# Kernel tuning notes

Measured on AMD Instinct MI355X. Metric: run time of the kernel, lower is better.

The kernel has to match this reference:

```python
import jax, jax.numpy as jnp
import numpy as np

QMAX = 127.0          # int8 symmetric range
MMA_ALPHA = 1024.0    # leap mmaAlpha; applied to one scale and removed from the other (net no-op)
EPS = 1e-12


def _dynamic_quantize(t):
    """Per-tensor (blockSize=-1) symmetric int8 dynamic quantization."""
    s = jnp.maximum(jnp.max(jnp.abs(t)) / QMAX, EPS)
    q = jnp.clip(jnp.round(t / s), -QMAX, QMAX).astype(jnp.int8)
    return q, s


def setup_inputs() -> dict:
    key = jax.random.key(0)
    k1, k2 = jax.random.split(key)
    x = jax.random.normal(k1, (8192, 256), dtype=jnp.float32)   # [M, K]
    y = jax.random.normal(k2, (256, 8192), dtype=jnp.float32)   # [K, N]
    return {"x": x, "y": y}


def reference(x, y):
    x_q, x_s = _dynamic_quantize(x)
    y_q, y_s = _dynamic_quantize(y)
    # Integer accumulation (K=256 * 127^2 fits easily in int32), then dequantize.
    acc = jnp.matmul(x_q.astype(jnp.int32), y_q.astype(jnp.int32))  # [M, N] int32
    # mmaAlpha rescaling: scale one operand's scale up by alpha, the other down; cancels exactly.
    out = acc.astype(jnp.float32) * ((x_s * MMA_ALPHA) * (y_s / MMA_ALPHA))
    return out
```

## Files before the change

### kernel.cpp

```cpp
#include <hip/hip_runtime.h>

#define M_DIM 8192
#define N_DIM 8192
#define K_DIM 256

typedef __attribute__((ext_vector_type(4))) int i32x4;
typedef __attribute__((ext_vector_type(4))) float f32x4;

__device__ __forceinline__ void bar_lds() {
    asm volatile("s_waitcnt lgkmcnt(0)" ::: "memory");
    __builtin_amdgcn_sched_barrier(0);
    __builtin_amdgcn_s_barrier();
}

__device__ __forceinline__ void bar_stage() {
    asm volatile("s_waitcnt vmcnt(0) lgkmcnt(0)" ::: "memory");
    __builtin_amdgcn_sched_barrier(0);
    __builtin_amdgcn_s_barrier();
}

__device__ __forceinline__ void async_lds16(const signed char* g, signed char* l) {
    __builtin_amdgcn_global_load_lds(
        (const __attribute__((address_space(1))) void*)g,
        (__attribute__((address_space(3))) void*)l, 16, 0, 0);
}

__global__ __launch_bounds__(256) void absmax_kernel(const float* __restrict__ x,
                                                     const float* __restrict__ y,
                                                     float* __restrict__ partial) {
    const float* p = (blockIdx.y == 0) ? x : y;
    const int n4 = (M_DIM * K_DIM) / 4;
    const float4* p4 = (const float4*)p;
    float m = 0.0f;
    for (int i = blockIdx.x * 256 + threadIdx.x; i < n4; i += 256 * 256) {
        float4 v = p4[i];
        m = fmaxf(m, fmaxf(fmaxf(fabsf(v.x), fabsf(v.y)), fmaxf(fabsf(v.z), fabsf(v.w))));
    }
    for (int off = 32; off > 0; off >>= 1)
        m = fmaxf(m, __shfl_down(m, off));
    __shared__ float sm[4];
    int wid = threadIdx.x >> 6;
    if ((threadIdx.x & 63) == 0) sm[wid] = m;
    __syncthreads();
    if (threadIdx.x == 0)
        partial[blockIdx.y * 256 + blockIdx.x] = fmaxf(fmaxf(sm[0], sm[1]), fmaxf(sm[2], sm[3]));
}

__device__ __forceinline__ void load_scales(const float* __restrict__ partial,
                                            float& sx, float& sy, float* ssc) {
    const int tid = threadIdx.x;
    float mx = partial[tid];
    float my = partial[256 + tid];
    for (int off = 32; off > 0; off >>= 1) {
        mx = fmaxf(mx, __shfl_down(mx, off));
        my = fmaxf(my, __shfl_down(my, off));
    }
    if ((tid & 63) == 0) { ssc[tid >> 6] = mx; ssc[4 + (tid >> 6)] = my; }
    __syncthreads();
    mx = fmaxf(fmaxf(ssc[0], ssc[1]), fmaxf(ssc[2], ssc[3]));
    my = fmaxf(fmaxf(ssc[4], ssc[5]), fmaxf(ssc[6], ssc[7]));
    sx = fmaxf(mx / 127.0f, 1e-12f);
    sy = fmaxf(my / 127.0f, 1e-12f);
}

__device__ __forceinline__ int quant1(float v, float s) {
    float q = rintf(v / s);
    q = fmaxf(-127.0f, fminf(127.0f, q));
    return (int)q;
}

__global__ __launch_bounds__(256) void quant_kernel(const float* __restrict__ x,
                                                    const float* __restrict__ y,
                                                    unsigned int* __restrict__ xq_w,
                                                    signed char* __restrict__ yqt,
                                                    const float* __restrict__ partial) {
    __shared__ float ssc[8];
    __shared__ signed char tile[64][68];
    float sx, sy;
    load_scales(partial, sx, sy, ssc);
    int b = blockIdx.x;
    const int t = threadIdx.x;
    if (b < 2048) {
        int i = b * 256 + t;
        float4 v = ((const float4*)x)[i];
        unsigned b0 = (unsigned)quant1(v.x, sx) & 0xFF;
        unsigned b1 = (unsigned)quant1(v.y, sx) & 0xFF;
        unsigned b2 = (unsigned)quant1(v.z, sx) & 0xFF;
        unsigned b3 = (unsigned)quant1(v.w, sx) & 0xFF;
        xq_w[i] = b0 | (b1 << 8) | (b2 << 16) | (b3 << 24);
    } else {
        b -= 2048;
        const int n0 = (b & 127) * 64;
        const int k0 = (b >> 7) * 64;
        #pragma unroll
        for (int r = 0; r < 16; ++r) {
            int idx = r * 256 + t;
            int k = idx >> 6, n = idx & 63;
            float v = y[(size_t)(k0 + k) * N_DIM + n0 + n];
            tile[k][n] = (signed char)quant1(v, sy);
        }
        __syncthreads();
        #pragma unroll
        for (int r = 0; r < 4; ++r) {
            int idx = r * 256 + t;
            int n = idx >> 4, kw = idx & 15;
            unsigned w = ((unsigned)(unsigned char)tile[kw * 4 + 0][n])
                       | ((unsigned)(unsigned char)tile[kw * 4 + 1][n] << 8)
                       | ((unsigned)(unsigned char)tile[kw * 4 + 2][n] << 16)
                       | ((unsigned)(unsigned char)tile[kw * 4 + 3][n] << 24);
            *(unsigned*)(yqt + (size_t)(n0 + n) * K_DIM + k0 + kw * 4) = w;
        }
    }
}

__global__ __launch_bounds__(256) void gemm_i8_kernel(const signed char* __restrict__ xq,
                                                      const signed char* __restrict__ yqt,
                                                      const float* __restrict__ partial,
                                                      float* __restrict__ out) {
    __shared__ __align__(16) unsigned char smem[32768];
    __shared__ float ssc[8];
    float (*epi)[132] = (float(*)[132])smem;

    float sx, sy;
    load_scales(partial, sx, sy, ssc);
    const float scale = (sx * 1024.0f) * (sy / 1024.0f);

    const int tid = threadIdx.x;
    const int w = tid >> 6;
    const int lane = tid & 63;
    const int wr = w >> 1, wc = w & 1;

    const signed char* gbase = (w < 2)
        ? (xq  + (size_t)(blockIdx.y * 128 + (w & 1) * 64 + (lane >> 2)) * K_DIM + (lane & 3) * 16)
        : (yqt + (size_t)(blockIdx.x * 128 + (w & 1) * 64 + (lane >> 2)) * K_DIM + (lane & 3) * 16);
    const int loff = ((w < 2) ? 0 : 8192) + (w & 1) * 64 * 64;

    const int frow = lane & 15;
    const int fk = (lane >> 4) * 16;

    i32x4 acc[4][4] = {};

    #pragma unroll
    for (int c = 0; c < 4; ++c)
        async_lds16(gbase + (size_t)(c * 16) * K_DIM, (signed char*)smem + loff + c * 16 * 64);
    bar_stage();

    #pragma unroll
    for (int ks = 0; ks < 4; ++ks) {
        signed char* cur = (signed char*)smem + (ks & 1) * 16384;
        if (ks < 3) {
            signed char* nxt = (signed char*)smem + ((ks + 1) & 1) * 16384;
            #pragma unroll
            for (int c = 0; c < 4; ++c)
                async_lds16(gbase + (size_t)(c * 16) * K_DIM + (ks + 1) * 64,
                            nxt + loff + c * 16 * 64);
        }
        const signed char* ard = cur + (wr * 64 + frow) * 64 + fk;
        const signed char* brd = cur + 8192 + (wc * 64 + frow) * 64 + fk;
        i32x4 a[4], b[4];
        #pragma unroll
        for (int mi = 0; mi < 4; ++mi)
            a[mi] = *(const i32x4*)(ard + mi * 16 * 64);
        #pragma unroll
        for (int ni = 0; ni < 4; ++ni)
            b[ni] = *(const i32x4*)(brd + ni * 16 * 64);
        #pragma unroll
        for (int mi = 0; mi < 4; ++mi)
            #pragma unroll
            for (int ni = 0; ni < 4; ++ni)
                acc[mi][ni] = __builtin_amdgcn_mfma_i32_16x16x64_i8(a[mi], b[ni], acc[mi][ni], 0, 0, 0);
        bar_stage();
    }

    const int qrow = (lane >> 4) * 4;
    const int qcol = lane & 15;
    #pragma unroll
    for (int mi = 0; mi < 4; ++mi) {
        if (mi) bar_lds();
        #pragma unroll
        for (int ni = 0; ni < 4; ++ni)
            #pragma unroll
            for (int r = 0; r < 4; ++r)
                epi[wr * 16 + qrow + r][wc * 64 + ni * 16 + qcol] =
                    (float)acc[mi][ni][r] * scale;
        bar_lds();
        #pragma unroll
        for (int i = 0; i < 4; ++i) {
            int row = i * 8 + (tid >> 5);
            int col4 = tid & 31;
            f32x4 v = *(const f32x4*)&epi[row][col4 * 4];
            int grow = blockIdx.y * 128 + (row >> 4) * 64 + mi * 16 + (row & 15);
            int gcol = blockIdx.x * 128 + col4 * 4;
            __builtin_nontemporal_store(v, (f32x4*)&out[(size_t)grow * N_DIM + gcol]);
        }
    }
}

extern "C" void kernel_launch(void* const* d_in, const int* in_sizes, int n_in,
                              void* d_out, int out_size, void* d_ws, size_t ws_size,
                              hipStream_t stream) {
    const float* x = (const float*)d_in[0];
    const float* y = (const float*)d_in[1];
    float* out = (float*)d_out;

    unsigned char* ws = (unsigned char*)d_ws;
    float* partial = (float*)ws;
    signed char* xq = (signed char*)(ws + 4096);
    signed char* yqt = xq + (size_t)M_DIM * K_DIM;

    absmax_kernel<<<dim3(256, 2), 256, 0, stream>>>(x, y, partial);

    quant_kernel<<<2048 + 512, 256, 0, stream>>>(x, y, (unsigned int*)xq, yqt, partial);

    gemm_i8_kernel<<<dim3(N_DIM / 128, M_DIM / 128), 256, 0, stream>>>(xq, yqt, partial, out);
}
```

Measured before the change: 68.16 us.

## Fuse absmax, quantize and int8 GEMM into one cooperative persistent kernel

Replaces the three separate launches with a single cooperative kernel of 512 persistent blocks. The absmax, quantization and GEMM phases are separated by grid-wide syncs, and the GEMM phase loops over 8 output tiles per block. This removes two kernel launch gaps and the tail effects between kernels. In exchange it adds grid.sync costs and reduces GEMM parallelism to a fixed 2 blocks per CU, and it falls back to the old three-kernel path if the cooperative launch fails.

```diff
diff --git a/kernel.cpp b/kernel.cpp
--- a/kernel.cpp
+++ b/kernel.cpp
@@ -1,8 +1,12 @@
 #include <hip/hip_runtime.h>
+#include <hip/hip_cooperative_groups.h>
 
 #define M_DIM 8192
 #define N_DIM 8192
 #define K_DIM 256
+#define NBLK 512
+
+namespace cg = cooperative_groups;
 
 typedef __attribute__((ext_vector_type(4))) int i32x4;
 typedef __attribute__((ext_vector_type(4))) float f32x4;
@@ -23,6 +27,183 @@
     __builtin_amdgcn_global_load_lds(
         (const __attribute__((address_space(1))) void*)g,
         (__attribute__((address_space(3))) void*)l, 16, 0, 0);
+}
+
+__device__ __forceinline__ int quant1(float v, float s) {
+    float q = rintf(v / s);
+    q = fmaxf(-127.0f, fminf(127.0f, q));
+    return (int)q;
+}
+
+__global__ __launch_bounds__(256, 2) void fused_kernel(const float* __restrict__ x,
+                                                       const float* __restrict__ y,
+                                                       float* __restrict__ partial,
+                                                       signed char* __restrict__ xq,
+                                                       signed char* __restrict__ yqt,
+                                                       float* __restrict__ out) {
+    cg::grid_group grid = cg::this_grid();
+    __shared__ __align__(16) unsigned char smem[32768];
+    __shared__ float ssc[8];
+
+    const int tid = threadIdx.x;
+    const int bid = blockIdx.x;
+    const float4* x4 = (const float4*)x;
+    const float4* y4 = (const float4*)y;
+
+    {
+        float mx = 0.0f, my = 0.0f;
+        const int n4 = (M_DIM * K_DIM) / 4;
+        for (int i = bid * 256 + tid; i < n4; i += NBLK * 256) {
+            float4 v = x4[i];
+            mx = fmaxf(mx, fmaxf(fmaxf(fabsf(v.x), fabsf(v.y)), fmaxf(fabsf(v.z), fabsf(v.w))));
+            float4 u = y4[i];
+            my = fmaxf(my, fmaxf(fmaxf(fabsf(u.x), fabsf(u.y)), fmaxf(fabsf(u.z), fabsf(u.w))));
+        }
+        for (int off = 32; off > 0; off >>= 1) {
+            mx = fmaxf(mx, __shfl_down(mx, off));
+            my = fmaxf(my, __shfl_down(my, off));
+        }
+        if ((tid & 63) == 0) { ssc[tid >> 6] = mx; ssc[4 + (tid >> 6)] = my; }
+        __syncthreads();
+        if (tid == 0) {
+            partial[bid]        = fmaxf(fmaxf(ssc[0], ssc[1]), fmaxf(ssc[2], ssc[3]));
+            partial[NBLK + bid] = fmaxf(fmaxf(ssc[4], ssc[5]), fmaxf(ssc[6], ssc[7]));
+        }
+    }
+    grid.sync();
+
+    float sx, sy;
+    {
+        float mx = fmaxf(partial[tid], partial[tid + 256]);
+        float my = fmaxf(partial[NBLK + tid], partial[NBLK + tid + 256]);
+        for (int off = 32; off > 0; off >>= 1) {
+            mx = fmaxf(mx, __shfl_down(mx, off));
+            my = fmaxf(my, __shfl_down(my, off));
+        }
+        __syncthreads();
+        if ((tid & 63) == 0) { ssc[tid >> 6] = mx; ssc[4 + (tid >> 6)] = my; }
+        __syncthreads();
+        mx = fmaxf(fmaxf(ssc[0], ssc[1]), fmaxf(ssc[2], ssc[3]));
+        my = fmaxf(fmaxf(ssc[4], ssc[5]), fmaxf(ssc[6], ssc[7]));
+        sx = fmaxf(mx / 127.0f, 1e-12f);
+        sy = fmaxf(my / 127.0f, 1e-12f);
+    }
+
+    {
+        signed char (*tile)[68] = (signed char(*)[68])smem;
+        for (int u = bid; u < 2560; u += NBLK) {
+            if (u < 2048) {
+                int i = u * 256 + tid;
+                float4 v = x4[i];
+                unsigned b0 = (unsigned)quant1(v.x, sx) & 0xFF;
+                unsigned b1 = (unsigned)quant1(v.y, sx) & 0xFF;
+                unsigned b2 = (unsigned)quant1(v.z, sx) & 0xFF;
+                unsigned b3 = (unsigned)quant1(v.w, sx) & 0xFF;
+                ((unsigned*)xq)[i] = b0 | (b1 << 8) | (b2 << 16) | (b3 << 24);
+            } else {
+                int b = u - 2048;
+                const int n0 = (b & 127) * 64;
+                const int k0 = (b >> 7) * 64;
+                __syncthreads();
+                #pragma unroll
+                for (int r = 0; r < 16; ++r) {
+                    int idx = r * 256 + tid;
+                    int k = idx >> 6, n = idx & 63;
+                    float v = y[(size_t)(k0 + k) * N_DIM + n0 + n];
+                    tile[k][n] = (signed char)quant1(v, sy);
+                }
+                __syncthreads();
+                #pragma unroll
+                for (int r = 0; r < 4; ++r) {
+                    int idx = r * 256 + tid;
+                    int n = idx >> 4, kw = idx & 15;
+                    unsigned wv = ((unsigned)(unsigned char)tile[kw * 4 + 0][n])
+                                | ((unsigned)(unsigned char)tile[kw * 4 + 1][n] << 8)
+                                | ((unsigned)(unsigned char)tile[kw * 4 + 2][n] << 16)
+                                | ((unsigned)(unsigned char)tile[kw * 4 + 3][n] << 24);
+                    *(unsigned*)(yqt + (size_t)(n0 + n) * K_DIM + k0 + kw * 4) = wv;
+                }
+            }
+        }
+    }
+    grid.sync();
+
+    float (*epi)[132] = (float(*)[132])smem;
+    const float scale = (sx * 1024.0f) * (sy / 1024.0f);
+    const int w = tid >> 6;
+    const int lane = tid & 63;
+    const int wr = w >> 1, wc = w & 1;
+    const int frow = lane & 15;
+    const int fk = (lane >> 4) * 16;
+    const int loff = ((w < 2) ? 0 : 8192) + (w & 1) * 64 * 64;
+
+    for (int t = 0; t < 8; ++t) {
+        const int tile_id = bid + t * NBLK;
+        const int bx = tile_id & 63;
+        const int by = tile_id >> 6;
+
+        const signed char* gbase = (w < 2)
+            ? (xq  + (size_t)(by * 128 + (w & 1) * 64 + (lane >> 2)) * K_DIM + (lane & 3) * 16)
+            : (yqt + (size_t)(bx * 128 + (w & 1) * 64 + (lane >> 2)) * K_DIM + (lane & 3) * 16);
+
+        i32x4 acc[4][4] = {};
+
+        if (t) bar_lds();
+        #pragma unroll
+        for (int c = 0; c < 4; ++c)
+            async_lds16(gbase + (size_t)(c * 16) * K_DIM, (signed char*)smem + loff + c * 16 * 64);
+        bar_stage();
+
+        #pragma unroll
+        for (int ks = 0; ks < 4; ++ks) {
+            signed char* cur = (signed char*)smem + (ks & 1) * 16384;
+            if (ks < 3) {
+                signed char* nxt = (signed char*)smem + ((ks + 1) & 1) * 16384;
+                #pragma unroll
+                for (int c = 0; c < 4; ++c)
+                    async_lds16(gbase + (size_t)(c * 16) * K_DIM + (ks + 1) * 64,
+                                nxt + loff + c * 16 * 64);
+            }
+            const signed char* ard = cur + (wr * 64 + frow) * 64 + fk;
+            const signed char* brd = cur + 8192 + (wc * 64 + frow) * 64 + fk;
+            i32x4 a[4], b[4];
+            #pragma unroll
+            for (int mi = 0; mi < 4; ++mi)
+                a[mi] = *(const i32x4*)(ard + mi * 16 * 64);
+            #pragma unroll
+            for (int ni = 0; ni < 4; ++ni)
+                b[ni] = *(const i32x4*)(brd + ni * 16 * 64);
+            #pragma unroll
+            for (int mi = 0; mi < 4; ++mi)
+                #pragma unroll
+                for (int ni = 0; ni < 4; ++ni)
+                    acc[mi][ni] = __builtin_amdgcn_mfma_i32_16x16x64_i8(a[mi], b[ni], acc[mi][ni], 0, 0, 0);
+            bar_stage();
+        }
+
+        const int qrow = (lane >> 4) * 4;
+        const int qcol = lane & 15;
+        #pragma unroll
+        for (int mi = 0; mi < 4; ++mi) {
+            if (mi) bar_lds();
+            #pragma unroll
+            for (int ni = 0; ni < 4; ++ni)
+                #pragma unroll
+                for (int r = 0; r < 4; ++r)
+                    epi[wr * 16 + qrow + r][wc * 64 + ni * 16 + qcol] =
+                        (float)acc[mi][ni][r] * scale;
+            bar_lds();
+            #pragma unroll
+            for (int i = 0; i < 4; ++i) {
+                int row = i * 8 + (tid >> 5);
+                int col4 = tid & 31;
+                f32x4 v = *(const f32x4*)&epi[row][col4 * 4];
+                int grow = by * 128 + (row >> 4) * 64 + mi * 16 + (row & 15);
+                int gcol = bx * 128 + col4 * 4;
+                __builtin_nontemporal_store(v, (f32x4*)&out[(size_t)grow * N_DIM + gcol]);
+            }
+        }
+    }
 }
 
 __global__ __launch_bounds__(256) void absmax_kernel(const float* __restrict__ x,
@@ -61,12 +242,6 @@
     my = fmaxf(fmaxf(ssc[4], ssc[5]), fmaxf(ssc[6], ssc[7]));
     sx = fmaxf(mx / 127.0f, 1e-12f);
     sy = fmaxf(my / 127.0f, 1e-12f);
-}
-
-__device__ __forceinline__ int quant1(float v, float s) {
-    float q = rintf(v / s);
-    q = fmaxf(-127.0f, fminf(127.0f, q));
-    return (int)q;
 }
 
 __global__ __launch_bounds__(256) void quant_kernel(const float* __restrict__ x,
@@ -104,11 +279,11 @@
         for (int r = 0; r < 4; ++r) {
             int idx = r * 256 + t;
             int n = idx >> 4, kw = idx & 15;
-            unsigned w = ((unsigned)(unsigned char)tile[kw * 4 + 0][n])
-                       | ((unsigned)(unsigned char)tile[kw * 4 + 1][n] << 8)
-                       | ((unsigned)(unsigned char)tile[kw * 4 + 2][n] << 16)
-                       | ((unsigned)(unsigned char)tile[kw * 4 + 3][n] << 24);
-            *(unsigned*)(yqt + (size_t)(n0 + n) * K_DIM + k0 + kw * 4) = w;
+            unsigned wv = ((unsigned)(unsigned char)tile[kw * 4 + 0][n])
+                        | ((unsigned)(unsigned char)tile[kw * 4 + 1][n] << 8)
+                        | ((unsigned)(unsigned char)tile[kw * 4 + 2][n] << 16)
+                        | ((unsigned)(unsigned char)tile[kw * 4 + 3][n] << 24);
+            *(unsigned*)(yqt + (size_t)(n0 + n) * K_DIM + k0 + kw * 4) = wv;
         }
     }
 }
@@ -204,13 +379,17 @@
     float* out = (float*)d_out;
 
     unsigned char* ws = (unsigned char*)d_ws;
-    float* partial = (float*)ws;
-    signed char* xq = (signed char*)(ws + 4096);
+    float* partial  = (float*)ws;
+    float* partial2 = (float*)(ws + 8192);
+    signed char* xq = (signed char*)(ws + 16384);
     signed char* yqt = xq + (size_t)M_DIM * K_DIM;
 
-    absmax_kernel<<<dim3(256, 2), 256, 0, stream>>>(x, y, partial);
-
-    quant_kernel<<<2048 + 512, 256, 0, stream>>>(x, y, (unsigned int*)xq, yqt, partial);
-
-    gemm_i8_kernel<<<dim3(N_DIM / 128, M_DIM / 128), 256, 0, stream>>>(xq, yqt, partial, out);
-}
+    void* args[] = { (void*)&x, (void*)&y, (void*)&partial, (void*)&xq, (void*)&yqt, (void*)&out };
+    hipError_t err = hipLaunchCooperativeKernel((const void*)fused_kernel, dim3(NBLK),
+                                                dim3(256), args, 0, stream);
+    if (err != hipSuccess) {
+        absmax_kernel<<<dim3(256, 2), 256, 0, stream>>>(x, y, partial2);
+        quant_kernel<<<2048 + 512, 256, 0, stream>>>(x, y, (unsigned int*)xq, yqt, partial2);
+        gemm_i8_kernel<<<dim3(N_DIM / 128, M_DIM / 128), 256, 0, stream>>>(xq, yqt, partial2, out);
+    }
+}
```

New measurement: 165.2 us. 142% more time.
